# Optimization experiments

Hardware: AMD Instinct MI355X
Metric: run time of the kernel (lower is better)

## Reference

```python
import jax, jax.numpy as jnp
import numpy as np

UNITS = 512
DIM = 64
BATCH = 2048


def setup_inputs() -> dict:
    key = jax.random.key(0)
    kx, k1, k2 = jax.random.split(key, 3)
    # glorot_uniform limit for (units, dim)
    limit = float(np.sqrt(6.0 / (UNITS + DIM)))
    x = jax.random.normal(kx, (BATCH, DIM), dtype=jnp.float32)
    q1 = jax.random.uniform(k1, (UNITS, DIM), dtype=jnp.float32, minval=-limit, maxval=limit)
    q2 = jax.random.uniform(k2, (UNITS, DIM), dtype=jnp.float32, minval=-limit, maxval=limit)
    r = jnp.ones((UNITS,), dtype=jnp.float32)
    return {"x": x, "q1": q1, "q2": q2, "r": r}


def reference(x, q1, q2, r):
    n = x.shape[-1]
    q12 = q2 - q1                                   # (U, n)
    q12_norm = jnp.linalg.norm(q12, axis=1)         # (U,)
    # scalar projection coefficient: (x - q1) . q12  -> (B, U)
    s = jnp.einsum('bn,un->bu', x, q12) - jnp.sum(q1 * q12, axis=1)
    # projection vector k = (s / ||q12||) * q12  -> (B, U, n)
    kv = (s / q12_norm)[..., None] * q12[None, :, :]
    temp1 = jnp.sum(kv * q12, axis=-1)              # (B, U)
    k_norm = jnp.linalg.norm(kv, axis=-1)           # (B, U)
    temp2 = k_norm / q12_norm                       # (B, U)
    # branchless select replacing the scatter/gather mask logic:
    #   temp1 < 0            -> l = 1
    #   temp1>=0 & temp2<1   -> l = k_norm
    #   else                 -> l = 0
    l = jnp.where(temp1 < 0, 1.0, jnp.where(temp2 < 1, k_norm, 0.0))  # (B, U)
    center = l[..., None] * q1 + (1.0 - l)[..., None] * q2            # (B, U, n)
    d = x[:, None, :] - center                                        # (B, U, n)
    y = -jnp.sum(d * d, axis=-1) / (n * jnp.square(r))                # (B, U)
    return jnp.exp(y)  # activation='exponential'
```

## Files before the change

kernel.cpp:

```cpp
#include <hip/hip_runtime.h>

#define BATCH 2048
#define UNITS 512
#define DIM   64
#define TB    64
#define TU    32

typedef __attribute__((ext_vector_type(8))) short short8v;
typedef __attribute__((ext_vector_type(4))) float float4v;

__device__ __forceinline__ unsigned short f2bf(float f) {
  union { float f; unsigned u; } v; v.f = f;
  return (unsigned short)((v.u + 0x7FFFu + ((v.u >> 16) & 1u)) >> 16);
}

__device__ __forceinline__ int swz(int row, int k) {
  return (row * 64 + k) ^ ((row & 7) << 3);
}

extern "C" __global__ void __launch_bounds__(256, 2)
sausage_v4(const float* __restrict__ x, const float* __restrict__ q1,
           const float* __restrict__ q2, const float* __restrict__ r,
           float* __restrict__ out)
{
  __shared__ __align__(16) unsigned short sX [TB * 64];
  __shared__ __align__(16) unsigned short sQ1[TU * 64];
  __shared__ __align__(16) unsigned short sQ2[TU * 64];
  __shared__ float Lt[TU], Lqn[TU], Lw[TU], Lnn[TU], Lq2n[TU], Linv[TU];
  __shared__ float Lxn[TB];

  const int tid = threadIdx.x;
  const int b0  = blockIdx.x * TB;
  const int u0  = blockIdx.y * TU;

  if (tid < 128) {
    const int u   = tid >> 2;
    const int seg = tid & 3;
    const float* q1p = q1 + (size_t)(u0 + u) * DIM + seg * 16;
    const float* q2p = q2 + (size_t)(u0 + u) * DIM + seg * 16;
    float av[16], cv[16];
    #pragma unroll
    for (int j = 0; j < 4; ++j) {
      const float4 a4 = reinterpret_cast<const float4*>(q1p)[j];
      const float4 c4 = reinterpret_cast<const float4*>(q2p)[j];
      av[4*j+0] = a4.x; av[4*j+1] = a4.y; av[4*j+2] = a4.z; av[4*j+3] = a4.w;
      cv[4*j+0] = c4.x; cv[4*j+1] = c4.y; cv[4*j+2] = c4.z; cv[4*j+3] = c4.w;
    }
    float nn = 0.f, w = 0.f, q2n = 0.f;
    #pragma unroll
    for (int j = 0; j < 16; ++j) {
      const float d = cv[j] - av[j];
      nn  = fmaf(d, d, nn);
      w   = fmaf(cv[j], d, w);
      q2n = fmaf(cv[j], cv[j], q2n);
    }
    #pragma unroll
    for (int h = 0; h < 2; ++h) {
      union { unsigned short u16[8]; short8v v; } p1, p2;
      #pragma unroll
      for (int j = 0; j < 8; ++j) {
        p1.u16[j] = f2bf(av[8*h+j]);
        p2.u16[j] = f2bf(cv[8*h+j]);
      }
      const int idx = swz(u, seg * 16 + 8 * h);
      *reinterpret_cast<short8v*>(&sQ1[idx]) = p1.v;
      *reinterpret_cast<short8v*>(&sQ2[idx]) = p2.v;
    }
    nn  += __shfl_xor(nn, 1);  nn  += __shfl_xor(nn, 2);
    w   += __shfl_xor(w, 1);   w   += __shfl_xor(w, 2);
    q2n += __shfl_xor(q2n, 1); q2n += __shfl_xor(q2n, 2);
    if (seg == 0) {
      const float rv = r[u0 + u];
      Lt[u]   = w - nn;
      Lqn[u]  = sqrtf(nn);
      Lw[u]   = w;
      Lnn[u]  = nn;
      Lq2n[u] = q2n;
      Linv[u] = 1.0f / (64.0f * rv * rv);
    }
  } else {
    const int tt   = tid - 128;
    const int row  = tt >> 1;
    const int half = tt & 1;
    const float* xp = x + (size_t)(b0 + row) * DIM + half * 32;
    float v[32];
    #pragma unroll
    for (int j = 0; j < 8; ++j) {
      const float4 v4 = reinterpret_cast<const float4*>(xp)[j];
      v[4*j+0] = v4.x; v[4*j+1] = v4.y; v[4*j+2] = v4.z; v[4*j+3] = v4.w;
    }
    float xn = 0.f;
    #pragma unroll
    for (int j = 0; j < 32; ++j) xn = fmaf(v[j], v[j], xn);
    #pragma unroll
    for (int h = 0; h < 4; ++h) {
      union { unsigned short u16[8]; short8v v; } p;
      #pragma unroll
      for (int j = 0; j < 8; ++j) p.u16[j] = f2bf(v[8*h+j]);
      const int idx = swz(row, half * 32 + 8 * h);
      *reinterpret_cast<short8v*>(&sX[idx]) = p.v;
    }
    xn += __shfl_xor(xn, 1);
    if (half == 0) Lxn[row] = xn;
  }
  __syncthreads();

  const int lane = tid & 63;
  const int wid  = tid >> 6;
  const int wr   = wid >> 1;
  const int wc   = wid & 1;
  const int l15  = lane & 15;
  const int lk   = lane >> 4;
  const int kb   = lk * 8;

  short8v a_frag[2][2], b1_frag[2], b2_frag[2];
  const int urow = wc * 16 + l15;
  #pragma unroll
  for (int ks = 0; ks < 2; ++ks) {
    const int qi = swz(urow, ks * 32 + kb);
    b1_frag[ks] = *reinterpret_cast<const short8v*>(&sQ1[qi]);
    b2_frag[ks] = *reinterpret_cast<const short8v*>(&sQ2[qi]);
    #pragma unroll
    for (int mt = 0; mt < 2; ++mt) {
      const int mrow = wr * 32 + mt * 16 + l15;
      a_frag[mt][ks] = *reinterpret_cast<const short8v*>(&sX[swz(mrow, ks * 32 + kb)]);
    }
  }

  float4v acc1[2], acc2[2];
  #pragma unroll
  for (int mt = 0; mt < 2; ++mt) {
    acc1[mt] = (float4v){0.f, 0.f, 0.f, 0.f};
    acc2[mt] = (float4v){0.f, 0.f, 0.f, 0.f};
  }
  #pragma unroll
  for (int mt = 0; mt < 2; ++mt)
    #pragma unroll
    for (int ks = 0; ks < 2; ++ks) {
      acc1[mt] = __builtin_amdgcn_mfma_f32_16x16x32_bf16(a_frag[mt][ks], b1_frag[ks], acc1[mt], 0, 0, 0);
      acc2[mt] = __builtin_amdgcn_mfma_f32_16x16x32_bf16(a_frag[mt][ks], b2_frag[ks], acc2[mt], 0, 0, 0);
    }

  const float t_   = Lt[urow];
  const float qn_  = Lqn[urow];
  const float w_   = Lw[urow];
  const float nn_  = Lnn[urow];
  const float q2n_ = Lq2n[urow];
  const float inv_ = Linv[urow];

  #pragma unroll
  for (int mt = 0; mt < 2; ++mt) {
    const int rbase = wr * 32 + mt * 16 + lk * 4;
    #pragma unroll
    for (int j = 0; j < 4; ++j) {
      const float d1 = acc1[mt][j];
      const float d2 = acc2[mt][j];
      const float a  = d2 - d1;
      const float s  = a - t_;
      const float l  = (s < 0.0f) ? 1.0f : ((s < qn_) ? s : 0.0f);
      const float dsq = fmaf(-2.0f, d2, Lxn[rbase + j]) + q2n_
                      + 2.0f * l * (a - w_) + l * l * nn_;
      out[(size_t)(b0 + rbase + j) * UNITS + u0 + urow] = __expf(-dsq * inv_);
    }
  }
}

extern "C" void kernel_launch(void* const* d_in, const int* in_sizes, int n_in,
                              void* d_out, int out_size, void* d_ws, size_t ws_size,
                              hipStream_t stream) {
  const float* x  = (const float*)d_in[0];
  const float* q1 = (const float*)d_in[1];
  const float* q2 = (const float*)d_in[2];
  const float* r  = (const float*)d_in[3];
  float* out = (float*)d_out;
  (void)d_ws; (void)ws_size;
  dim3 grid(BATCH / TB, UNITS / TU);
  sausage_v4<<<grid, 256, 0, stream>>>(x, q1, q2, r, out);
}
```

Before: 11.51 us.

## Load MFMA fragments directly from global into registers, single-wave blocks

Replaces the 256-thread block that staged bf16 tiles through swizzled shared memory with a 64-thread single-wave block. Each lane loads its MFMA fragment elements straight from global memory and packs them to bf16 in registers. Row norms are reduced with cross-lane shuffles. This removes the shared-memory staging, the block barrier and the LDS reads, and the grid grows to 64x32 small blocks. In exchange, each block covers a 32x16 output tile, so q and x are reloaded from global memory more often and stores are less coalesced per block.

After: 11.08 us. 3.7% less time.

```diff
diff --git a/kernel.cpp b/kernel.cpp
--- a/kernel.cpp
+++ b/kernel.cpp
@@ -3,8 +3,6 @@
 #define BATCH 2048
 #define UNITS 512
 #define DIM   64
-#define TB    64
-#define TU    32
 
 typedef __attribute__((ext_vector_type(8))) short short8v;
 typedef __attribute__((ext_vector_type(4))) float float4v;
@@ -14,143 +12,100 @@
   return (unsigned short)((v.u + 0x7FFFu + ((v.u >> 16) & 1u)) >> 16);
 }
 
-__device__ __forceinline__ int swz(int row, int k) {
-  return (row * 64 + k) ^ ((row & 7) << 3);
+__device__ __forceinline__ short8v pack8(const float* s) {
+  union { unsigned short u16[8]; short8v v; } p;
+  #pragma unroll
+  for (int j = 0; j < 8; ++j) p.u16[j] = f2bf(s[j]);
+  return p.v;
 }
 
-extern "C" __global__ void __launch_bounds__(256, 2)
-sausage_v4(const float* __restrict__ x, const float* __restrict__ q1,
+extern "C" __global__ void __launch_bounds__(64, 2)
+sausage_v5(const float* __restrict__ x, const float* __restrict__ q1,
            const float* __restrict__ q2, const float* __restrict__ r,
            float* __restrict__ out)
 {
-  __shared__ __align__(16) unsigned short sX [TB * 64];
-  __shared__ __align__(16) unsigned short sQ1[TU * 64];
-  __shared__ __align__(16) unsigned short sQ2[TU * 64];
-  __shared__ float Lt[TU], Lqn[TU], Lw[TU], Lnn[TU], Lq2n[TU], Linv[TU];
-  __shared__ float Lxn[TB];
+  const int lane = threadIdx.x;
+  const int l15  = lane & 15;
+  const int lk   = lane >> 4;
+  const int b0   = blockIdx.x * 32;
+  const int u0   = blockIdx.y * 16;
 
-  const int tid = threadIdx.x;
-  const int b0  = blockIdx.x * TB;
-  const int u0  = blockIdx.y * TU;
-
-  if (tid < 128) {
-    const int u   = tid >> 2;
-    const int seg = tid & 3;
-    const float* q1p = q1 + (size_t)(u0 + u) * DIM + seg * 16;
-    const float* q2p = q2 + (size_t)(u0 + u) * DIM + seg * 16;
-    float av[16], cv[16];
+  float q1f[16], q2f[16], xf[2][16];
+  {
+    const float* q1r = q1 + (size_t)(u0 + l15) * DIM + lk * 8;
+    const float* q2r = q2 + (size_t)(u0 + l15) * DIM + lk * 8;
     #pragma unroll
-    for (int j = 0; j < 4; ++j) {
-      const float4 a4 = reinterpret_cast<const float4*>(q1p)[j];
-      const float4 c4 = reinterpret_cast<const float4*>(q2p)[j];
-      av[4*j+0] = a4.x; av[4*j+1] = a4.y; av[4*j+2] = a4.z; av[4*j+3] = a4.w;
-      cv[4*j+0] = c4.x; cv[4*j+1] = c4.y; cv[4*j+2] = c4.z; cv[4*j+3] = c4.w;
-    }
-    float nn = 0.f, w = 0.f, q2n = 0.f;
-    #pragma unroll
-    for (int j = 0; j < 16; ++j) {
-      const float d = cv[j] - av[j];
-      nn  = fmaf(d, d, nn);
-      w   = fmaf(cv[j], d, w);
-      q2n = fmaf(cv[j], cv[j], q2n);
+    for (int ks = 0; ks < 2; ++ks) {
+      *(float4*)&q1f[8*ks + 0] = *(const float4*)(q1r + ks * 32);
+      *(float4*)&q1f[8*ks + 4] = *(const float4*)(q1r + ks * 32 + 4);
+      *(float4*)&q2f[8*ks + 0] = *(const float4*)(q2r + ks * 32);
+      *(float4*)&q2f[8*ks + 4] = *(const float4*)(q2r + ks * 32 + 4);
     }
     #pragma unroll
-    for (int h = 0; h < 2; ++h) {
-      union { unsigned short u16[8]; short8v v; } p1, p2;
+    for (int mt = 0; mt < 2; ++mt) {
+      const float* xr = x + (size_t)(b0 + mt * 16 + l15) * DIM + lk * 8;
       #pragma unroll
-      for (int j = 0; j < 8; ++j) {
-        p1.u16[j] = f2bf(av[8*h+j]);
-        p2.u16[j] = f2bf(cv[8*h+j]);
+      for (int ks = 0; ks < 2; ++ks) {
+        *(float4*)&xf[mt][8*ks + 0] = *(const float4*)(xr + ks * 32);
+        *(float4*)&xf[mt][8*ks + 4] = *(const float4*)(xr + ks * 32 + 4);
       }
-      const int idx = swz(u, seg * 16 + 8 * h);
-      *reinterpret_cast<short8v*>(&sQ1[idx]) = p1.v;
-      *reinterpret_cast<short8v*>(&sQ2[idx]) = p2.v;
     }
-    nn  += __shfl_xor(nn, 1);  nn  += __shfl_xor(nn, 2);
-    w   += __shfl_xor(w, 1);   w   += __shfl_xor(w, 2);
-    q2n += __shfl_xor(q2n, 1); q2n += __shfl_xor(q2n, 2);
-    if (seg == 0) {
-      const float rv = r[u0 + u];
-      Lt[u]   = w - nn;
-      Lqn[u]  = sqrtf(nn);
-      Lw[u]   = w;
-      Lnn[u]  = nn;
-      Lq2n[u] = q2n;
-      Linv[u] = 1.0f / (64.0f * rv * rv);
-    }
-  } else {
-    const int tt   = tid - 128;
-    const int row  = tt >> 1;
-    const int half = tt & 1;
-    const float* xp = x + (size_t)(b0 + row) * DIM + half * 32;
-    float v[32];
-    #pragma unroll
-    for (int j = 0; j < 8; ++j) {
-      const float4 v4 = reinterpret_cast<const float4*>(xp)[j];
-      v[4*j+0] = v4.x; v[4*j+1] = v4.y; v[4*j+2] = v4.z; v[4*j+3] = v4.w;
-    }
-    float xn = 0.f;
-    #pragma unroll
-    for (int j = 0; j < 32; ++j) xn = fmaf(v[j], v[j], xn);
-    #pragma unroll
-    for (int h = 0; h < 4; ++h) {
-      union { unsigned short u16[8]; short8v v; } p;
-      #pragma unroll
-      for (int j = 0; j < 8; ++j) p.u16[j] = f2bf(v[8*h+j]);
-      const int idx = swz(row, half * 32 + 8 * h);
-      *reinterpret_cast<short8v*>(&sX[idx]) = p.v;
-    }
-    xn += __shfl_xor(xn, 1);
-    if (half == 0) Lxn[row] = xn;
   }
-  __syncthreads();
+  const float rv = r[u0 + l15];
 
-  const int lane = tid & 63;
-  const int wid  = tid >> 6;
-  const int wr   = wid >> 1;
-  const int wc   = wid & 1;
-  const int l15  = lane & 15;
-  const int lk   = lane >> 4;
-  const int kb   = lk * 8;
+  float nn = 0.f, w = 0.f, q2n = 0.f;
+  #pragma unroll
+  for (int j = 0; j < 16; ++j) {
+    const float d = q2f[j] - q1f[j];
+    nn  = fmaf(d, d, nn);
+    w   = fmaf(q2f[j], d, w);
+    q2n = fmaf(q2f[j], q2f[j], q2n);
+  }
+  float xnp0 = 0.f, xnp1 = 0.f;
+  #pragma unroll
+  for (int j = 0; j < 16; ++j) {
+    xnp0 = fmaf(xf[0][j], xf[0][j], xnp0);
+    xnp1 = fmaf(xf[1][j], xf[1][j], xnp1);
+  }
+  nn   += __shfl_xor(nn, 16);   nn   += __shfl_xor(nn, 32);
+  w    += __shfl_xor(w, 16);    w    += __shfl_xor(w, 32);
+  q2n  += __shfl_xor(q2n, 16);  q2n  += __shfl_xor(q2n, 32);
+  xnp0 += __shfl_xor(xnp0, 16); xnp0 += __shfl_xor(xnp0, 32);
+  xnp1 += __shfl_xor(xnp1, 16); xnp1 += __shfl_xor(xnp1, 32);
 
-  short8v a_frag[2][2], b1_frag[2], b2_frag[2];
-  const int urow = wc * 16 + l15;
+  const float t_   = w - nn;
+  const float qn_  = sqrtf(nn);
+  const float inv_ = 1.0f / (64.0f * rv * rv);
+
+  short8v b1_frag[2], b2_frag[2], a_frag[2][2];
   #pragma unroll
   for (int ks = 0; ks < 2; ++ks) {
-    const int qi = swz(urow, ks * 32 + kb);
-    b1_frag[ks] = *reinterpret_cast<const short8v*>(&sQ1[qi]);
-    b2_frag[ks] = *reinterpret_cast<const short8v*>(&sQ2[qi]);
-    #pragma unroll
-    for (int mt = 0; mt < 2; ++mt) {
-      const int mrow = wr * 32 + mt * 16 + l15;
-      a_frag[mt][ks] = *reinterpret_cast<const short8v*>(&sX[swz(mrow, ks * 32 + kb)]);
-    }
+    b1_frag[ks] = pack8(&q1f[8 * ks]);
+    b2_frag[ks] = pack8(&q2f[8 * ks]);
+    a_frag[0][ks] = pack8(&xf[0][8 * ks]);
+    a_frag[1][ks] = pack8(&xf[1][8 * ks]);
   }
-
   float4v acc1[2], acc2[2];
   #pragma unroll
   for (int mt = 0; mt < 2; ++mt) {
     acc1[mt] = (float4v){0.f, 0.f, 0.f, 0.f};
     acc2[mt] = (float4v){0.f, 0.f, 0.f, 0.f};
-  }
-  #pragma unroll
-  for (int mt = 0; mt < 2; ++mt)
     #pragma unroll
     for (int ks = 0; ks < 2; ++ks) {
       acc1[mt] = __builtin_amdgcn_mfma_f32_16x16x32_bf16(a_frag[mt][ks], b1_frag[ks], acc1[mt], 0, 0, 0);
       acc2[mt] = __builtin_amdgcn_mfma_f32_16x16x32_bf16(a_frag[mt][ks], b2_frag[ks], acc2[mt], 0, 0, 0);
     }
+  }
 
-  const float t_   = Lt[urow];
-  const float qn_  = Lqn[urow];
-  const float w_   = Lw[urow];
-  const float nn_  = Lnn[urow];
-  const float q2n_ = Lq2n[urow];
-  const float inv_ = Linv[urow];
+  float xnv[2][4];
+  #pragma unroll
+  for (int j = 0; j < 4; ++j) {
+    xnv[0][j] = __shfl(xnp0, lk * 4 + j);
+    xnv[1][j] = __shfl(xnp1, lk * 4 + j);
+  }
 
   #pragma unroll
   for (int mt = 0; mt < 2; ++mt) {
-    const int rbase = wr * 32 + mt * 16 + lk * 4;
     #pragma unroll
     for (int j = 0; j < 4; ++j) {
       const float d1 = acc1[mt][j];
@@ -158,9 +113,10 @@
       const float a  = d2 - d1;
       const float s  = a - t_;
       const float l  = (s < 0.0f) ? 1.0f : ((s < qn_) ? s : 0.0f);
-      const float dsq = fmaf(-2.0f, d2, Lxn[rbase + j]) + q2n_
-                      + 2.0f * l * (a - w_) + l * l * nn_;
-      out[(size_t)(b0 + rbase + j) * UNITS + u0 + urow] = __expf(-dsq * inv_);
+      const float dsq = fmaf(-2.0f, d2, xnv[mt][j]) + q2n
+                      + 2.0f * l * (a - w) + l * l * nn;
+      const int row = b0 + mt * 16 + lk * 4 + j;
+      out[(size_t)row * UNITS + u0 + l15] = __expf(-dsq * inv_);
     }
   }
 }
@@ -174,6 +130,6 @@
   const float* r  = (const float*)d_in[3];
   float* out = (float*)d_out;
   (void)d_ws; (void)ws_size;
-  dim3 grid(BATCH / TB, UNITS / TU);
-  sausage_v4<<<grid, 256, 0, stream>>>(x, q1, q2, r, out);
+  dim3 grid(BATCH / 32, UNITS / 16);
+  sausage_v5<<<grid, 64, 0, stream>>>(x, q1, q2, r, out);
 }
```
